# Performance work log

Hardware: AMD Instinct MI355X
Metric: run time of the kernel (lower is better)

Reference implementation:

```python
import jax, jax.numpy as jnp
import numpy as np

D_MODEL = 1024
D_STATE = 16
D_CONV = 4
EXPAND = 2
D_INNER = D_MODEL * EXPAND
BATCH = 4
SEQLEN = 4096


def setup_inputs() -> dict:
    key = jax.random.key(0)
    ks = jax.random.split(key, 10)
    s = 1.0 / np.sqrt(D_MODEL)
    si = 1.0 / np.sqrt(D_INNER)
    return {
        "x": jax.random.normal(ks[0], (BATCH, SEQLEN, D_MODEL), jnp.float32),
        "x_proj_w": jax.random.normal(ks[1], (D_INNER, D_MODEL), jnp.float32) * s,
        "dt_proj_w": jax.random.normal(ks[2], (D_INNER, D_MODEL), jnp.float32) * s,
        "dt_proj_b": jax.random.normal(ks[3], (D_INNER,), jnp.float32) * 0.1,
        "A_log": jax.random.normal(ks[4], (D_INNER, D_STATE), jnp.float32),
        "D": jnp.ones((D_INNER,), jnp.float32),
        "B_proj_w": jax.random.normal(ks[5], (D_STATE, D_MODEL), jnp.float32) * s,
        "C_proj_w": jax.random.normal(ks[6], (D_STATE, D_MODEL), jnp.float32) * s,
        "conv_w": jax.random.normal(ks[7], (D_INNER, 1, D_CONV), jnp.float32) * 0.5,
        "conv_b": jax.random.normal(ks[8], (D_INNER,), jnp.float32) * 0.1,
        "out_proj_w": jax.random.normal(ks[9], (D_MODEL, D_INNER), jnp.float32) * si,
    }


def _selective_scan(xc, delta, A, B, C, D):
    # xc, delta: (b, L, d_inner); B, C: (b, L, d_state); A: (d_inner, d_state)
    batch, seqlen, d_inner = xc.shape
    d_state = A.shape[1]

    def step(h, inp):
        x_t, dt, B_t, C_t = inp  # (b,di), (b,di), (b,ds), (b,ds)
        A_disc = jnp.exp(dt[:, :, None] * A[None])           # (b, di, ds)
        h = A_disc * h + (dt[:, :, None] * B_t[:, None, :]) * x_t[:, :, None]
        y_t = jnp.einsum('bds,bs->bd', h, C_t) + D[None, :] * x_t
        return h, y_t

    h0 = jnp.zeros((batch, d_inner, d_state), xc.dtype)
    xs = (jnp.swapaxes(xc, 0, 1), jnp.swapaxes(delta, 0, 1),
          jnp.swapaxes(B, 0, 1), jnp.swapaxes(C, 0, 1))
    _, ys = jax.lax.scan(step, h0, xs)  # ys: (L, b, d_inner)
    return jnp.swapaxes(ys, 0, 1)


def reference(x, x_proj_w, dt_proj_w, dt_proj_b, A_log, D, B_proj_w, C_proj_w, conv_w, conv_b, out_proj_w):
    seqlen = x.shape[1]
    x_inner = x @ x_proj_w.T  # (b, L, d_inner)
    # causal depthwise conv1d: torch pads both sides by d_conv-1 then keeps first L,
    # equivalent to left-pad (d_conv-1, 0)
    xc = jax.lax.conv_general_dilated(
        jnp.swapaxes(x_inner, 1, 2), conv_w,
        window_strides=(1,), padding=[(D_CONV - 1, 0)],
        dimension_numbers=('NCH', 'OIH', 'NCH'),
        feature_group_count=D_INNER)
    xc = jnp.swapaxes(xc + conv_b[None, :, None], 1, 2)
    xc = jax.nn.silu(xc)
    B = x @ B_proj_w.T
    C = x @ C_proj_w.T
    delta = jax.nn.softplus(x @ dt_proj_w.T + dt_proj_b)
    A = -jnp.exp(A_log.astype(jnp.float32))
    y = _selective_scan(xc, delta, A, B, C, D)
    return y @ out_proj_w.T
```

## Files before the change

### kernel.cpp

```cpp
#include <hip/hip_runtime.h>
#include <hip/hip_bf16.h>
#include <math.h>

typedef __bf16 bf16;
typedef __bf16 bf16x2 __attribute__((ext_vector_type(2)));
typedef __bf16 bf16x8 __attribute__((ext_vector_type(8)));
typedef float f32x4 __attribute__((ext_vector_type(4)));

#define AS_G __attribute__((address_space(1)))
#define AS_L __attribute__((address_space(3)))

#define NCHUNK 64
#define CLEN   64

__device__ __forceinline__ void async_ld16(const void* g, void* l) {
  __builtin_amdgcn_global_load_lds((const AS_G void*)g, (AS_L void*)l, 16, 0, 0);
}
__device__ __forceinline__ float fexp2(float x) { return __builtin_amdgcn_exp2f(x); }

__global__ void detect_dtype(const void* __restrict__ Dones, int* __restrict__ flag) {
  if (threadIdx.x == 0 && blockIdx.x == 0) {
    *flag = (*(const unsigned int*)Dones == 0x3F803F80u) ? 0 : 1;
  }
}

__global__ __launch_bounds__(256) void to_bf16(
    const void* __restrict__ src, bf16* __restrict__ dst, int n8,
    const int* __restrict__ flag)
{
  const int i = blockIdx.x * 256 + threadIdx.x;
  if (i >= n8) return;
  bf16x8 o;
  if (*flag) {
    const f32x4* s = (const f32x4*)src;
    f32x4 a = s[2*i], b = s[2*i + 1];
    #pragma unroll
    for (int e = 0; e < 4; ++e) { o[e] = (bf16)a[e]; o[e+4] = (bf16)b[e]; }
  } else {
    o = ((const bf16x8*)src)[i];
  }
  ((bf16x8*)dst)[i] = o;
}

template<int EPI>
__global__ __launch_bounds__(256, 2) void gemm_bt(
    const bf16* __restrict__ A, const bf16* __restrict__ W,
    bf16* __restrict__ OutB, float* __restrict__ OutF,
    const bf16* __restrict__ bias, const int* __restrict__ flag,
    int M, int N, int K)
{
  __shared__ bf16 smA[2][128*32];
  __shared__ bf16 smB[2][128*32];
  const int tid  = threadIdx.x;
  const int wave = tid >> 6;
  const int lane = tid & 63;
  const int m0 = blockIdx.x * 128;
  const int n0 = blockIdx.y * 128;
  const int wm = (wave >> 1) * 64;
  const int wn = (wave & 1) * 64;
  const int lm = lane & 15;
  const int q  = lane >> 4;
  const bool f32o = (EPI == 2) && (*flag != 0);

  f32x4 acc[4][4] = {};

  const int chunk0 = wave*128 + lane;
  const int chunk1 = chunk0 + 64;
  const int r0 = chunk0 >> 2, c0 = chunk0 & 3;
  const int r1 = chunk1 >> 2, c1 = chunk1 & 3;
  const int sc0 = c0 ^ ((r0 >> 1) & 3);
  const int sc1 = c1 ^ ((r1 >> 1) & 3);
  const bf16* gA0 = A + (size_t)(m0 + r0)*K + sc0*8;
  const bf16* gA1 = A + (size_t)(m0 + r1)*K + sc1*8;
  const bf16* gB0 = W + (size_t)(n0 + r0)*K + sc0*8;
  const bf16* gB1 = W + (size_t)(n0 + r1)*K + sc1*8;
  const int oA0 = (wave*128     )*8;
  const int oA1 = (wave*128 + 64)*8;

  auto stage = [&](int buf, int k0) {
    async_ld16(gA0 + k0, &smA[buf][oA0]);
    async_ld16(gA1 + k0, &smA[buf][oA1]);
    async_ld16(gB0 + k0, &smB[buf][oA0]);
    async_ld16(gB1 + k0, &smB[buf][oA1]);
  };

  const int sl = (q ^ ((lm >> 1) & 3)) * 8;

  auto compute = [&](const bf16* sA, const bf16* sB) {
    bf16x8 af[4], bfr[4];
    #pragma unroll
    for (int mi = 0; mi < 4; ++mi)
      af[mi] = *(const bf16x8*)(sA + (wm + mi*16 + lm)*32 + sl);
    #pragma unroll
    for (int ni = 0; ni < 4; ++ni)
      bfr[ni] = *(const bf16x8*)(sB + (wn + ni*16 + lm)*32 + sl);
    #pragma unroll
    for (int mi = 0; mi < 4; ++mi)
      #pragma unroll
      for (int ni = 0; ni < 4; ++ni)
        acc[mi][ni] = __builtin_amdgcn_mfma_f32_16x16x32_bf16(af[mi], bfr[ni], acc[mi][ni], 0, 0, 0);
  };

  stage(0, 0);
  __syncthreads();

  for (int k0 = 0; k0 < K; k0 += 64) {
    stage(1, k0 + 32);
    compute(smA[0], smB[0]);
    __syncthreads();
    if (k0 + 64 < K) stage(0, k0 + 64);
    compute(smA[1], smB[1]);
    __syncthreads();
  }

  #pragma unroll
  for (int mi = 0; mi < 4; ++mi) {
    #pragma unroll
    for (int ni = 0; ni < 4; ++ni) {
      const int col = n0 + wn + ni*16 + lm;
      float bval = 0.f;
      if (EPI == 1) bval = (float)bias[col];
      #pragma unroll
      for (int r = 0; r < 4; ++r) {
        const int row = m0 + wm + mi*16 + q*4 + r;
        float v = acc[mi][ni][r];
        if (EPI == 1) {
          v += bval;
          v = (v > 20.f) ? v : __logf(1.f + __expf(v));
        }
        const size_t idx = (size_t)row*N + col;
        if (EPI == 2 && f32o) OutF[idx] = v;
        else                  OutB[idx] = (bf16)v;
      }
    }
  }
}

__global__ __launch_bounds__(64) void bc_gemm(
    const bf16* __restrict__ X,
    const bf16* __restrict__ Bw, const bf16* __restrict__ Cw,
    float* __restrict__ Bout, float* __restrict__ Cout)
{
  const int lane = threadIdx.x;
  const int lm = lane & 15, q = lane >> 4;
  const int m0 = blockIdx.x * 16;
  const bf16* W = blockIdx.y ? Cw : Bw;
  float* O      = blockIdx.y ? Cout : Bout;
  f32x4 acc = {};
  const bf16* pa = X + (size_t)(m0 + lm)*1024 + q*8;
  const bf16* pw = W + (size_t)lm*1024 + q*8;
  for (int k0 = 0; k0 < 1024; k0 += 32) {
    bf16x8 a = *(const bf16x8*)(pa + k0);
    bf16x8 w = *(const bf16x8*)(pw + k0);
    acc = __builtin_amdgcn_mfma_f32_16x16x32_bf16(a, w, acc, 0, 0, 0);
  }
  #pragma unroll
  for (int r = 0; r < 4; ++r)
    O[(size_t)(m0 + q*4 + r)*16 + lm] = acc[r];
}

__global__ __launch_bounds__(256) void conv_silu(
    const bf16* __restrict__ Xin, const bf16* __restrict__ cw,
    const bf16* __restrict__ cb, bf16* __restrict__ Xc)
{
  const int idx = blockIdx.x * 256 + threadIdx.x;
  const int row = idx >> 8;
  const int dv  = (idx & 255) * 8;
  const int t   = row & 4095;
  bf16x8 wv[4];
  const bf16x8* pw = (const bf16x8*)(cw + (size_t)dv*4);
  #pragma unroll
  for (int j = 0; j < 4; ++j) wv[j] = pw[j];
  bf16x8 bv = *(const bf16x8*)(cb + dv);
  float acc[8];
  #pragma unroll
  for (int e = 0; e < 8; ++e) acc[e] = (float)bv[e];
  #pragma unroll
  for (int j = 0; j < 4; ++j) {
    const int tr = t - 3 + j;
    if (tr < 0) continue;
    bf16x8 xv = *(const bf16x8*)(Xin + (size_t)(row - 3 + j)*2048 + dv);
    #pragma unroll
    for (int e = 0; e < 8; ++e) {
      const int li = e*4 + j;
      acc[e] += (float)xv[e] * (float)wv[li >> 3][li & 7];
    }
  }
  bf16x8 o;
  #pragma unroll
  for (int e = 0; e < 8; ++e) {
    float v = acc[e];
    v = v / (1.f + __expf(-v));
    o[e] = (bf16)v;
  }
  *(bf16x8*)(Xc + (size_t)row*2048 + dv) = o;
}

__global__ __launch_bounds__(256) void scan_phase1(
    const bf16* __restrict__ Xc, const bf16* __restrict__ Dt,
    const float* __restrict__ Bm, const bf16* __restrict__ A_log,
    float* __restrict__ Hend, float* __restrict__ Dtsum)
{
  const int tid = threadIdx.x;
  const int d0 = blockIdx.x * 512 + tid * 2;
  const int c = blockIdx.y;
  const int b = blockIdx.z;
  const int t0 = c * CLEN;
  __shared__ float sB[CLEN*16];
  {
    const f32x4* src = (const f32x4*)(Bm + ((size_t)b*4096 + t0)*16);
    ((f32x4*)sB)[tid] = src[tid];
  }
  __syncthreads();
  float A2[2][16];
  {
    bf16x8 av[4];
    const bf16x8* pA = (const bf16x8*)(A_log + (size_t)d0*16);
    #pragma unroll
    for (int j = 0; j < 4; ++j) av[j] = pA[j];
    #pragma unroll
    for (int u = 0; u < 2; ++u)
      #pragma unroll
      for (int s = 0; s < 16; ++s) {
        const int li = u*16 + s;
        A2[u][s] = -__expf((float)av[li >> 3][li & 7]) * 1.44269504088896f;
      }
  }
  float h[2][16] = {};
  float dts[2] = {0.f, 0.f};
  const bf16* pX = Xc + ((size_t)b*4096 + t0)*2048 + d0;
  const bf16* pD = Dt + ((size_t)b*4096 + t0)*2048 + d0;
  bf16x2 vD = *(const bf16x2*)pD;
  bf16x2 vX = *(const bf16x2*)pX;
  for (int t = 0; t < CLEN; ++t) {
    bf16x2 nD = vD, nX = vX;
    if (t < CLEN-1) {
      nD = *(const bf16x2*)(pD + (size_t)(t+1)*2048);
      nX = *(const bf16x2*)(pX + (size_t)(t+1)*2048);
    }
    f32x4 Bv[4];
    #pragma unroll
    for (int i = 0; i < 4; ++i) Bv[i] = ((const f32x4*)(sB + t*16))[i];
    #pragma unroll
    for (int u = 0; u < 2; ++u) {
      const float dt = (float)vD[u];
      const float xv = (float)vX[u];
      dts[u] += dt;
      const float dx = dt * xv;
      #pragma unroll
      for (int s = 0; s < 16; ++s) {
        const float ad = fexp2(dt * A2[u][s]);
        h[u][s] = ad*h[u][s] + dx * Bv[s>>2][s&3];
      }
    }
    vD = nD; vX = nX;
  }
  #pragma unroll
  for (int u = 0; u < 2; ++u) {
    const size_t base = (((size_t)b*NCHUNK + c)*2048 + d0 + u)*16;
    #pragma unroll
    for (int s = 0; s < 16; ++s) Hend[base + s] = h[u][s];
    Dtsum[((size_t)b*NCHUNK + c)*2048 + d0 + u] = dts[u];
  }
}

__global__ __launch_bounds__(256) void scan_phase2(
    float* __restrict__ H,
    const float* __restrict__ Dtsum,
    const bf16* __restrict__ A_log)
{
  const int idx = blockIdx.x*256 + threadIdx.x;
  const int s = idx & 15;
  const int d = (idx >> 4) & 2047;
  const int b = idx >> 15;
  const float A2 = -__expf((float)A_log[d*16 + s]) * 1.44269504088896f;
  float h = 0.f;
  for (int c = 0; c < NCHUNK; ++c) {
    const size_t off = (((size_t)b*NCHUNK + c)*2048 + d)*16 + s;
    const float hend = H[off];
    H[off] = h;
    const float ap = fexp2(A2 * Dtsum[((size_t)b*NCHUNK + c)*2048 + d]);
    h = h*ap + hend;
  }
}

__global__ __launch_bounds__(256) void scan_phase3(
    const bf16* __restrict__ Xc, const bf16* __restrict__ Dt,
    const float* __restrict__ Bm, const float* __restrict__ Cm,
    const bf16* __restrict__ A_log, const bf16* __restrict__ Dvec,
    const float* __restrict__ Hstart, bf16* __restrict__ Y)
{
  const int tid = threadIdx.x;
  const int d0 = blockIdx.x * 512 + tid * 2;
  const int c = blockIdx.y;
  const int b = blockIdx.z;
  const int t0 = c * CLEN;
  __shared__ float sB[CLEN*16];
  __shared__ float sC[CLEN*16];
  {
    const f32x4* srcB = (const f32x4*)(Bm + ((size_t)b*4096 + t0)*16);
    const f32x4* srcC = (const f32x4*)(Cm + ((size_t)b*4096 + t0)*16);
    ((f32x4*)sB)[tid] = srcB[tid];
    ((f32x4*)sC)[tid] = srcC[tid];
  }
  __syncthreads();
  float A2[2][16];
  {
    bf16x8 av[4];
    const bf16x8* pA = (const bf16x8*)(A_log + (size_t)d0*16);
    #pragma unroll
    for (int j = 0; j < 4; ++j) av[j] = pA[j];
    #pragma unroll
    for (int u = 0; u < 2; ++u)
      #pragma unroll
      for (int s = 0; s < 16; ++s) {
        const int li = u*16 + s;
        A2[u][s] = -__expf((float)av[li >> 3][li & 7]) * 1.44269504088896f;
      }
  }
  float h[2][16];
  #pragma unroll
  for (int u = 0; u < 2; ++u) {
    const size_t base = (((size_t)b*NCHUNK + c)*2048 + d0 + u)*16;
    #pragma unroll
    for (int s = 0; s < 16; ++s) h[u][s] = Hstart[base + s];
  }
  const float Dd0 = (float)Dvec[d0];
  const float Dd1 = (float)Dvec[d0 + 1];
  const bf16* pX = Xc + ((size_t)b*4096 + t0)*2048 + d0;
  const bf16* pD = Dt + ((size_t)b*4096 + t0)*2048 + d0;
  bf16*       pY = Y  + ((size_t)b*4096 + t0)*2048 + d0;
  bf16x2 vD = *(const bf16x2*)pD;
  bf16x2 vX = *(const bf16x2*)pX;
  for (int t = 0; t < CLEN; ++t) {
    bf16x2 nD = vD, nX = vX;
    if (t < CLEN-1) {
      nD = *(const bf16x2*)(pD + (size_t)(t+1)*2048);
      nX = *(const bf16x2*)(pX + (size_t)(t+1)*2048);
    }
    f32x4 Bv[4], Cv[4];
    #pragma unroll
    for (int i = 0; i < 4; ++i) {
      Bv[i] = ((const f32x4*)(sB + t*16))[i];
      Cv[i] = ((const f32x4*)(sC + t*16))[i];
    }
    float y[2];
    #pragma unroll
    for (int u = 0; u < 2; ++u) {
      const float dt = (float)vD[u];
      const float xv = (float)vX[u];
      const float dx = dt * xv;
      float yp[4] = {0.f, 0.f, 0.f, 0.f};
      #pragma unroll
      for (int s = 0; s < 16; ++s) {
        const float ad = fexp2(dt * A2[u][s]);
        h[u][s] = ad*h[u][s] + dx * Bv[s>>2][s&3];
        yp[s & 3] += h[u][s] * Cv[s>>2][s&3];
      }
      y[u] = ((yp[0] + yp[1]) + (yp[2] + yp[3])) + (u ? Dd1 : Dd0) * xv;
    }
    bf16x2 yo; yo[0] = (bf16)y[0]; yo[1] = (bf16)y[1];
    *(bf16x2*)(pY + (size_t)t*2048) = yo;
    vD = nD; vX = nX;
  }
}

extern "C" void kernel_launch(void* const* d_in, const int* in_sizes, int n_in,
                              void* d_out, int out_size, void* d_ws, size_t ws_size,
                              hipStream_t stream)
{
  char* ws = (char*)d_ws;
  size_t off = 0;
  auto alloc = [&](size_t bytes) -> char* {
    char* p = ws + off; off += (bytes + 255) & ~(size_t)255; return p;
  };
  bf16*  xin = (bf16*) alloc((size_t)16384*2048*2);
  bf16*  dlt = (bf16*) alloc((size_t)16384*2048*2);
  bf16*  xc  = (bf16*) alloc((size_t)16384*2048*2);
  float* Bm  = (float*)alloc((size_t)16384*16*4);
  float* Cm  = (float*)alloc((size_t)16384*16*4);
  int*   flag = (int*) alloc(256);
  const int ncanon = 11;
  static const int canon_n[11] = {
    4*4096*1024, 2048*1024, 2048*1024, 2048, 2048*16, 2048,
    16*1024, 16*1024, 2048*4, 2048, 1024*2048 };
  bf16* canon[11];
  for (int i = 0; i < ncanon; ++i) canon[i] = (bf16*)alloc((size_t)canon_n[i]*2);
  float* Hst = (float*)canon[0];
  float* Dts = (float*)canon[1];
  if (off > ws_size) return;

  detect_dtype<<<1, 64, 0, stream>>>(d_in[5], flag);
  for (int i = 0; i < ncanon; ++i) {
    const int n8 = canon_n[i] / 8;
    to_bf16<<<(n8 + 255)/256, 256, 0, stream>>>(d_in[i], canon[i], n8, flag);
  }
  const bf16* x          = canon[0];
  const bf16* x_proj_w   = canon[1];
  const bf16* dt_proj_w  = canon[2];
  const bf16* dt_proj_b  = canon[3];
  const bf16* A_log      = canon[4];
  const bf16* Dvec       = canon[5];
  const bf16* B_proj_w   = canon[6];
  const bf16* C_proj_w   = canon[7];
  const bf16* conv_w     = canon[8];
  const bf16* conv_b     = canon[9];
  const bf16* out_proj_w = canon[10];

  gemm_bt<0><<<dim3(128,16), 256, 0, stream>>>(x, x_proj_w,  xin, nullptr, nullptr,   flag, 16384, 2048, 1024);
  gemm_bt<1><<<dim3(128,16), 256, 0, stream>>>(x, dt_proj_w, dlt, nullptr, dt_proj_b, flag, 16384, 2048, 1024);
  bc_gemm<<<dim3(1024,2), 64, 0, stream>>>(x, B_proj_w, C_proj_w, Bm, Cm);
  conv_silu<<<dim3(16384), 256, 0, stream>>>(xin, conv_w, conv_b, xc);
  scan_phase1<<<dim3(4,NCHUNK,4), 256, 0, stream>>>(xc, dlt, Bm, A_log, Hst, Dts);
  scan_phase2<<<dim3(512),        256, 0, stream>>>(Hst, Dts, A_log);
  scan_phase3<<<dim3(4,NCHUNK,4), 256, 0, stream>>>(xc, dlt, Bm, Cm, A_log, Dvec, Hst, xin );
  gemm_bt<2><<<dim3(128,8), 256, 0, stream>>>(xin, out_proj_w, (bf16*)d_out, (float*)d_out, nullptr, flag, 16384, 1024, 2048);
}
```

Before: 658.3 us.

## Assign one channel per thread in chunked scan and transpose state layout

The chunked scan kernels now give each thread one channel instead of two, doubling the grid and adding an occupancy hint of 8 blocks per SM. This halves per-thread registers and doubles the number of independent threads available to hide exp and FMA latency. The chunk-state buffer is transposed to [b][chunk][state][channel], so per-state stores, loads and the phase-2 recurrence are coalesced across channels. In exchange, per-thread loads shrink to scalar bf16 and the explicit next-step prefetch of dt/x is dropped.

```diff
diff --git a/kernel.cpp b/kernel.cpp
--- a/kernel.cpp
+++ b/kernel.cpp
@@ -196,13 +196,13 @@
   *(bf16x8*)(Xc + (size_t)row*2048 + dv) = o;
 }
 
-__global__ __launch_bounds__(256) void scan_phase1(
+__global__ __launch_bounds__(256, 8) void scan_phase1(
     const bf16* __restrict__ Xc, const bf16* __restrict__ Dt,
     const float* __restrict__ Bm, const bf16* __restrict__ A_log,
     float* __restrict__ Hend, float* __restrict__ Dtsum)
 {
   const int tid = threadIdx.x;
-  const int d0 = blockIdx.x * 512 + tid * 2;
+  const int d0 = blockIdx.x * 256 + tid;
   const int c = blockIdx.y;
   const int b = blockIdx.z;
   const int t0 = c * CLEN;
@@ -212,56 +212,37 @@
     ((f32x4*)sB)[tid] = src[tid];
   }
   __syncthreads();
-  float A2[2][16];
-  {
-    bf16x8 av[4];
+  float A2[16];
+  {
+    bf16x8 av[2];
     const bf16x8* pA = (const bf16x8*)(A_log + (size_t)d0*16);
-    #pragma unroll
-    for (int j = 0; j < 4; ++j) av[j] = pA[j];
-    #pragma unroll
-    for (int u = 0; u < 2; ++u)
-      #pragma unroll
-      for (int s = 0; s < 16; ++s) {
-        const int li = u*16 + s;
-        A2[u][s] = -__expf((float)av[li >> 3][li & 7]) * 1.44269504088896f;
-      }
-  }
-  float h[2][16] = {};
-  float dts[2] = {0.f, 0.f};
+    av[0] = pA[0]; av[1] = pA[1];
+    #pragma unroll
+    for (int s = 0; s < 16; ++s)
+      A2[s] = -__expf((float)av[s >> 3][s & 7]) * 1.44269504088896f;
+  }
+  float h[16] = {};
+  float dts = 0.f;
   const bf16* pX = Xc + ((size_t)b*4096 + t0)*2048 + d0;
   const bf16* pD = Dt + ((size_t)b*4096 + t0)*2048 + d0;
-  bf16x2 vD = *(const bf16x2*)pD;
-  bf16x2 vX = *(const bf16x2*)pX;
   for (int t = 0; t < CLEN; ++t) {
-    bf16x2 nD = vD, nX = vX;
-    if (t < CLEN-1) {
-      nD = *(const bf16x2*)(pD + (size_t)(t+1)*2048);
-      nX = *(const bf16x2*)(pX + (size_t)(t+1)*2048);
-    }
+    const float dt = (float)pD[(size_t)t*2048];
+    const float xv = (float)pX[(size_t)t*2048];
+    dts += dt;
+    const float dx = dt * xv;
     f32x4 Bv[4];
     #pragma unroll
     for (int i = 0; i < 4; ++i) Bv[i] = ((const f32x4*)(sB + t*16))[i];
     #pragma unroll
-    for (int u = 0; u < 2; ++u) {
-      const float dt = (float)vD[u];
-      const float xv = (float)vX[u];
-      dts[u] += dt;
-      const float dx = dt * xv;
-      #pragma unroll
-      for (int s = 0; s < 16; ++s) {
-        const float ad = fexp2(dt * A2[u][s]);
-        h[u][s] = ad*h[u][s] + dx * Bv[s>>2][s&3];
-      }
-    }
-    vD = nD; vX = nX;
-  }
-  #pragma unroll
-  for (int u = 0; u < 2; ++u) {
-    const size_t base = (((size_t)b*NCHUNK + c)*2048 + d0 + u)*16;
-    #pragma unroll
-    for (int s = 0; s < 16; ++s) Hend[base + s] = h[u][s];
-    Dtsum[((size_t)b*NCHUNK + c)*2048 + d0 + u] = dts[u];
-  }
+    for (int s = 0; s < 16; ++s) {
+      const float ad = fexp2(dt * A2[s]);
+      h[s] = ad*h[s] + dx * Bv[s>>2][s&3];
+    }
+  }
+  const size_t base = ((size_t)b*NCHUNK + c)*16;
+  #pragma unroll
+  for (int s = 0; s < 16; ++s) Hend[(base + s)*2048 + d0] = h[s];
+  Dtsum[((size_t)b*NCHUNK + c)*2048 + d0] = dts;
 }
 
 __global__ __launch_bounds__(256) void scan_phase2(
@@ -270,13 +251,13 @@
     const bf16* __restrict__ A_log)
 {
   const int idx = blockIdx.x*256 + threadIdx.x;
-  const int s = idx & 15;
-  const int d = (idx >> 4) & 2047;
+  const int d = idx & 2047;
+  const int s = (idx >> 11) & 15;
   const int b = idx >> 15;
   const float A2 = -__expf((float)A_log[d*16 + s]) * 1.44269504088896f;
   float h = 0.f;
   for (int c = 0; c < NCHUNK; ++c) {
-    const size_t off = (((size_t)b*NCHUNK + c)*2048 + d)*16 + s;
+    const size_t off = (((size_t)b*NCHUNK + c)*16 + s)*2048 + d;
     const float hend = H[off];
     H[off] = h;
     const float ap = fexp2(A2 * Dtsum[((size_t)b*NCHUNK + c)*2048 + d]);
@@ -284,14 +265,14 @@
   }
 }
 
-__global__ __launch_bounds__(256) void scan_phase3(
+__global__ __launch_bounds__(256, 8) void scan_phase3(
     const bf16* __restrict__ Xc, const bf16* __restrict__ Dt,
     const float* __restrict__ Bm, const float* __restrict__ Cm,
     const bf16* __restrict__ A_log, const bf16* __restrict__ Dvec,
     const float* __restrict__ Hstart, bf16* __restrict__ Y)
 {
   const int tid = threadIdx.x;
-  const int d0 = blockIdx.x * 512 + tid * 2;
+  const int d0 = blockIdx.x * 256 + tid;
   const int c = blockIdx.y;
   const int b = blockIdx.z;
   const int t0 = c * CLEN;
@@ -304,64 +285,44 @@
     ((f32x4*)sC)[tid] = srcC[tid];
   }
   __syncthreads();
-  float A2[2][16];
-  {
-    bf16x8 av[4];
+  float A2[16];
+  {
+    bf16x8 av[2];
     const bf16x8* pA = (const bf16x8*)(A_log + (size_t)d0*16);
-    #pragma unroll
-    for (int j = 0; j < 4; ++j) av[j] = pA[j];
-    #pragma unroll
-    for (int u = 0; u < 2; ++u)
-      #pragma unroll
-      for (int s = 0; s < 16; ++s) {
-        const int li = u*16 + s;
-        A2[u][s] = -__expf((float)av[li >> 3][li & 7]) * 1.44269504088896f;
-      }
-  }
-  float h[2][16];
-  #pragma unroll
-  for (int u = 0; u < 2; ++u) {
-    const size_t base = (((size_t)b*NCHUNK + c)*2048 + d0 + u)*16;
-    #pragma unroll
-    for (int s = 0; s < 16; ++s) h[u][s] = Hstart[base + s];
-  }
-  const float Dd0 = (float)Dvec[d0];
-  const float Dd1 = (float)Dvec[d0 + 1];
+    av[0] = pA[0]; av[1] = pA[1];
+    #pragma unroll
+    for (int s = 0; s < 16; ++s)
+      A2[s] = -__expf((float)av[s >> 3][s & 7]) * 1.44269504088896f;
+  }
+  float h[16];
+  {
+    const size_t base = ((size_t)b*NCHUNK + c)*16;
+    #pragma unroll
+    for (int s = 0; s < 16; ++s) h[s] = Hstart[(base + s)*2048 + d0];
+  }
+  const float Dd = (float)Dvec[d0];
   const bf16* pX = Xc + ((size_t)b*4096 + t0)*2048 + d0;
   const bf16* pD = Dt + ((size_t)b*4096 + t0)*2048 + d0;
   bf16*       pY = Y  + ((size_t)b*4096 + t0)*2048 + d0;
-  bf16x2 vD = *(const bf16x2*)pD;
-  bf16x2 vX = *(const bf16x2*)pX;
   for (int t = 0; t < CLEN; ++t) {
-    bf16x2 nD = vD, nX = vX;
-    if (t < CLEN-1) {
-      nD = *(const bf16x2*)(pD + (size_t)(t+1)*2048);
-      nX = *(const bf16x2*)(pX + (size_t)(t+1)*2048);
-    }
+    const float dt = (float)pD[(size_t)t*2048];
+    const float xv = (float)pX[(size_t)t*2048];
+    const float dx = dt * xv;
     f32x4 Bv[4], Cv[4];
     #pragma unroll
     for (int i = 0; i < 4; ++i) {
       Bv[i] = ((const f32x4*)(sB + t*16))[i];
       Cv[i] = ((const f32x4*)(sC + t*16))[i];
     }
-    float y[2];
-    #pragma unroll
-    for (int u = 0; u < 2; ++u) {
-      const float dt = (float)vD[u];
-      const float xv = (float)vX[u];
-      const float dx = dt * xv;
-      float yp[4] = {0.f, 0.f, 0.f, 0.f};
-      #pragma unroll
-      for (int s = 0; s < 16; ++s) {
-        const float ad = fexp2(dt * A2[u][s]);
-        h[u][s] = ad*h[u][s] + dx * Bv[s>>2][s&3];
-        yp[s & 3] += h[u][s] * Cv[s>>2][s&3];
-      }
-      y[u] = ((yp[0] + yp[1]) + (yp[2] + yp[3])) + (u ? Dd1 : Dd0) * xv;
-    }
-    bf16x2 yo; yo[0] = (bf16)y[0]; yo[1] = (bf16)y[1];
-    *(bf16x2*)(pY + (size_t)t*2048) = yo;
-    vD = nD; vX = nX;
+    float yp[4] = {0.f, 0.f, 0.f, 0.f};
+    #pragma unroll
+    for (int s = 0; s < 16; ++s) {
+      const float ad = fexp2(dt * A2[s]);
+      h[s] = ad*h[s] + dx * Bv[s>>2][s&3];
+      yp[s & 3] += h[s] * Cv[s>>2][s&3];
+    }
+    const float y = ((yp[0] + yp[1]) + (yp[2] + yp[3])) + Dd * xv;
+    pY[(size_t)t*2048] = (bf16)y;
   }
 }
 
@@ -411,8 +372,8 @@
   gemm_bt<1><<<dim3(128,16), 256, 0, stream>>>(x, dt_proj_w, dlt, nullptr, dt_proj_b, flag, 16384, 2048, 1024);
   bc_gemm<<<dim3(1024,2), 64, 0, stream>>>(x, B_proj_w, C_proj_w, Bm, Cm);
   conv_silu<<<dim3(16384), 256, 0, stream>>>(xin, conv_w, conv_b, xc);
-  scan_phase1<<<dim3(4,NCHUNK,4), 256, 0, stream>>>(xc, dlt, Bm, A_log, Hst, Dts);
+  scan_phase1<<<dim3(8,NCHUNK,4), 256, 0, stream>>>(xc, dlt, Bm, A_log, Hst, Dts);
   scan_phase2<<<dim3(512),        256, 0, stream>>>(Hst, Dts, A_log);
-  scan_phase3<<<dim3(4,NCHUNK,4), 256, 0, stream>>>(xc, dlt, Bm, Cm, A_log, Dvec, Hst, xin );
+  scan_phase3<<<dim3(8,NCHUNK,4), 256, 0, stream>>>(xc, dlt, Bm, Cm, A_log, Dvec, Hst, xin );
   gemm_bt<2><<<dim3(128,8), 256, 0, stream>>>(xin, out_proj_w, (bf16*)d_out, (float*)d_out, nullptr, flag, 16384, 1024, 2048);
 }
```

After: 668.7 us. No clear change (+1.6%).

## Enlarge GEMM tiles to 256x256 with triple-buffered async LDS pipeline

Applied to the files above, without the earlier changes.

Replaces the 128x128, 256-thread GEMM with a 256x256 tile run by 512 threads, where each wave computes 128x64. Staging moves from double to triple buffering with explicit vmcnt waits and raw barriers, and MFMA priority is raised with s_setprio. Block x indices are swizzled so blocks sharing the same tiles run close together. The goal is more data reuse per LDS load, fewer global loads and better overlap of loads with compute, at the cost of more registers (32 accumulators per lane), more LDS and fewer blocks, which may hurt occupancy and wave balance.

```diff
diff --git a/kernel.cpp b/kernel.cpp
--- a/kernel.cpp
+++ b/kernel.cpp
@@ -43,78 +43,96 @@
 }
 
 template<int EPI>
-__global__ __launch_bounds__(256, 2) void gemm_bt(
+__global__ __launch_bounds__(512, 2) void gemm_bt2(
     const bf16* __restrict__ A, const bf16* __restrict__ W,
     bf16* __restrict__ OutB, float* __restrict__ OutF,
     const bf16* __restrict__ bias, const int* __restrict__ flag,
     int M, int N, int K)
 {
-  __shared__ bf16 smA[2][128*32];
-  __shared__ bf16 smB[2][128*32];
+  __shared__ bf16 smA[3][256*32];
+  __shared__ bf16 smB[3][256*32];
   const int tid  = threadIdx.x;
   const int wave = tid >> 6;
   const int lane = tid & 63;
-  const int m0 = blockIdx.x * 128;
-  const int n0 = blockIdx.y * 128;
-  const int wm = (wave >> 1) * 64;
-  const int wn = (wave & 1) * 64;
+  const int bx  = blockIdx.x;
+  const int cpx = gridDim.x >> 3;
+  const int bxs = (bx & 7) * cpx + (bx >> 3);
+  const int m0 = bxs * 256;
+  const int n0 = blockIdx.y * 256;
+  const int wm = (wave >> 2) * 128;
+  const int wn = (wave & 3) * 64;
   const int lm = lane & 15;
   const int q  = lane >> 4;
   const bool f32o = (EPI == 2) && (*flag != 0);
 
-  f32x4 acc[4][4] = {};
-
-  const int chunk0 = wave*128 + lane;
-  const int chunk1 = chunk0 + 64;
-  const int r0 = chunk0 >> 2, c0 = chunk0 & 3;
-  const int r1 = chunk1 >> 2, c1 = chunk1 & 3;
-  const int sc0 = c0 ^ ((r0 >> 1) & 3);
-  const int sc1 = c1 ^ ((r1 >> 1) & 3);
+  f32x4 acc[8][4] = {};
+
+  const int c0i = tid;
+  const int c1i = tid + 512;
+  const int r0 = c0i >> 2, cc0 = c0i & 3;
+  const int r1 = c1i >> 2, cc1 = c1i & 3;
+  const int sc0 = cc0 ^ ((r0 >> 1) & 3);
+  const int sc1 = cc1 ^ ((r1 >> 1) & 3);
   const bf16* gA0 = A + (size_t)(m0 + r0)*K + sc0*8;
   const bf16* gA1 = A + (size_t)(m0 + r1)*K + sc1*8;
   const bf16* gB0 = W + (size_t)(n0 + r0)*K + sc0*8;
   const bf16* gB1 = W + (size_t)(n0 + r1)*K + sc1*8;
-  const int oA0 = (wave*128     )*8;
-  const int oA1 = (wave*128 + 64)*8;
+  const int o0 = c0i * 8;
+  const int o1 = c1i * 8;
 
   auto stage = [&](int buf, int k0) {
-    async_ld16(gA0 + k0, &smA[buf][oA0]);
-    async_ld16(gA1 + k0, &smA[buf][oA1]);
-    async_ld16(gB0 + k0, &smB[buf][oA0]);
-    async_ld16(gB1 + k0, &smB[buf][oA1]);
+    async_ld16(gA0 + k0, &smA[buf][o0]);
+    async_ld16(gA1 + k0, &smA[buf][o1]);
+    async_ld16(gB0 + k0, &smB[buf][o0]);
+    async_ld16(gB1 + k0, &smB[buf][o1]);
   };
 
   const int sl = (q ^ ((lm >> 1) & 3)) * 8;
 
-  auto compute = [&](const bf16* sA, const bf16* sB) {
-    bf16x8 af[4], bfr[4];
-    #pragma unroll
-    for (int mi = 0; mi < 4; ++mi)
+  const int nt = K >> 5;
+  stage(0, 0);
+  stage(1, 32);
+
+  for (int t = 0; t < nt; ++t) {
+    const int buf = t % 3;
+    if (t + 2 < nt) {
+      stage((t + 2) % 3, (t + 2) * 32);
+      asm volatile("s_waitcnt vmcnt(8)" ::: "memory");
+    } else if (t + 1 < nt) {
+      asm volatile("s_waitcnt vmcnt(4)" ::: "memory");
+    } else {
+      asm volatile("s_waitcnt vmcnt(0)" ::: "memory");
+    }
+    __builtin_amdgcn_sched_barrier(0);
+    __builtin_amdgcn_s_barrier();
+    __builtin_amdgcn_sched_barrier(0);
+
+    const bf16* sA = smA[buf];
+    const bf16* sB = smB[buf];
+    bf16x8 af[8], bfr[4];
+    #pragma unroll
+    for (int mi = 0; mi < 8; ++mi)
       af[mi] = *(const bf16x8*)(sA + (wm + mi*16 + lm)*32 + sl);
     #pragma unroll
     for (int ni = 0; ni < 4; ++ni)
       bfr[ni] = *(const bf16x8*)(sB + (wn + ni*16 + lm)*32 + sl);
-    #pragma unroll
-    for (int mi = 0; mi < 4; ++mi)
+
+    __builtin_amdgcn_s_setprio(1);
+    #pragma unroll
+    for (int mi = 0; mi < 8; ++mi)
       #pragma unroll
       for (int ni = 0; ni < 4; ++ni)
         acc[mi][ni] = __builtin_amdgcn_mfma_f32_16x16x32_bf16(af[mi], bfr[ni], acc[mi][ni], 0, 0, 0);
-  };
-
-  stage(0, 0);
-  __syncthreads();
-
-  for (int k0 = 0; k0 < K; k0 += 64) {
-    stage(1, k0 + 32);
-    compute(smA[0], smB[0]);
-    __syncthreads();
-    if (k0 + 64 < K) stage(0, k0 + 64);
-    compute(smA[1], smB[1]);
-    __syncthreads();
-  }
-
-  #pragma unroll
-  for (int mi = 0; mi < 4; ++mi) {
+    __builtin_amdgcn_s_setprio(0);
+
+    asm volatile("s_waitcnt lgkmcnt(0)" ::: "memory");
+    __builtin_amdgcn_sched_barrier(0);
+    __builtin_amdgcn_s_barrier();
+    __builtin_amdgcn_sched_barrier(0);
+  }
+
+  #pragma unroll
+  for (int mi = 0; mi < 8; ++mi) {
     #pragma unroll
     for (int ni = 0; ni < 4; ++ni) {
       const int col = n0 + wn + ni*16 + lm;
@@ -407,12 +425,12 @@
   const bf16* conv_b     = canon[9];
   const bf16* out_proj_w = canon[10];
 
-  gemm_bt<0><<<dim3(128,16), 256, 0, stream>>>(x, x_proj_w,  xin, nullptr, nullptr,   flag, 16384, 2048, 1024);
-  gemm_bt<1><<<dim3(128,16), 256, 0, stream>>>(x, dt_proj_w, dlt, nullptr, dt_proj_b, flag, 16384, 2048, 1024);
+  gemm_bt2<0><<<dim3(64,8), 512, 0, stream>>>(x, x_proj_w,  xin, nullptr, nullptr,   flag, 16384, 2048, 1024);
+  gemm_bt2<1><<<dim3(64,8), 512, 0, stream>>>(x, dt_proj_w, dlt, nullptr, dt_proj_b, flag, 16384, 2048, 1024);
   bc_gemm<<<dim3(1024,2), 64, 0, stream>>>(x, B_proj_w, C_proj_w, Bm, Cm);
   conv_silu<<<dim3(16384), 256, 0, stream>>>(xin, conv_w, conv_b, xc);
   scan_phase1<<<dim3(4,NCHUNK,4), 256, 0, stream>>>(xc, dlt, Bm, A_log, Hst, Dts);
   scan_phase2<<<dim3(512),        256, 0, stream>>>(Hst, Dts, A_log);
   scan_phase3<<<dim3(4,NCHUNK,4), 256, 0, stream>>>(xc, dlt, Bm, Cm, A_log, Dvec, Hst, xin );
-  gemm_bt<2><<<dim3(128,8), 256, 0, stream>>>(xin, out_proj_w, (bf16*)d_out, (float*)d_out, nullptr, flag, 16384, 1024, 2048);
-}
+  gemm_bt2<2><<<dim3(64,4), 512, 0, stream>>>(xin, out_proj_w, (bf16*)d_out, (float*)d_out, nullptr, flag, 16384, 1024, 2048);
+}
```

New measurement: 675.6 us. 2.6% more time.
